# Kernel optimization log

Hardware: AMD Instinct MI355X
Metric: run time of the kernel (lower is better)

Reference implementation:

```python
import jax, jax.numpy as jnp
import numpy as np

P, N, M = 4, 8192, 8192

def setup_inputs() -> dict:
    key = jax.random.key(0)
    k1, k2, k3, k4, k5 = jax.random.split(key, 5)
    return {
        "camera_pts": jax.random.normal(k1, (P, N, 3), dtype=jnp.float32),
        "cad_pts": jax.random.normal(k2, (P, M, 3), dtype=jnp.float32),
        "part_weight": jax.random.uniform(k3, (P,), dtype=jnp.float32),
        "rot_quat": jax.random.normal(k4, (P, 4), dtype=jnp.float32),
        "tra": jax.random.normal(k5, (P, 3, 1), dtype=jnp.float32),
    }

def _quat_to_rot(q):
    # q: [P,4] in (w,x,y,z) order, normalized outside
    a, b, c, d = q[:, 0], q[:, 1], q[:, 2], q[:, 3]
    rows = jnp.stack([
        1 - 2*c*c - 2*d*d, 2*b*c - 2*a*d,     2*a*c + 2*b*d,
        2*b*c + 2*a*d,     1 - 2*b*b - 2*d*d, 2*c*d - 2*a*b,
        2*b*d - 2*a*c,     2*a*b + 2*c*d,     1 - 2*b*b - 2*c*c,
    ], axis=-1)  # [P,9]
    return rows.reshape(-1, 3, 3)

def _chamfer(x, y):
    # x: [N,4], y: [M,4] -> scalar bidirectional chamfer (Euclidean, not squared)
    x2 = jnp.sum(x * x, axis=-1)              # [N]
    y2 = jnp.sum(y * y, axis=-1)              # [M]
    d2 = x2[:, None] + y2[None, :] - 2.0 * (x @ y.T)
    dist = jnp.sqrt(jnp.clip(d2, 0.0))        # [N,M]
    return jnp.mean(jnp.min(dist, axis=1)) + jnp.mean(jnp.min(dist, axis=0))

def reference(camera_pts, cad_pts, part_weight, rot_quat, tra):
    q = rot_quat / jnp.linalg.norm(rot_quat, axis=1, keepdims=True)
    rot = _quat_to_rot(q)                                       # [P,3,3]
    top = jnp.concatenate([rot, tra], axis=2)                   # [P,3,4]
    bottom = jnp.broadcast_to(jnp.array([[[0.0, 0.0, 0.0, 1.0]]], dtype=rot.dtype), (rot.shape[0], 1, 4))
    transforms = jnp.concatenate([top, bottom], axis=1)         # [P,4,4]
    ones_cad = jnp.ones(cad_pts.shape[:-1] + (1,), dtype=cad_pts.dtype)
    ones_cam = jnp.ones(camera_pts.shape[:-1] + (1,), dtype=camera_pts.dtype)
    cad_h = jnp.concatenate([cad_pts, ones_cad], axis=-1)       # [P,M,4]
    cam_h = jnp.concatenate([camera_pts, ones_cam], axis=-1)    # [P,N,4]
    cad_base = jnp.einsum('pij,pmj->pmi', transforms, cad_h)    # [P,M,4]
    cd = jax.vmap(_chamfer)(cad_base, cam_h)                    # [P]
    all_objective = jnp.sum(part_weight * cd)
    return all_objective, jax.lax.stop_gradient(transforms)
```

## Files before the change

kernel.cpp:

```cpp
#include <hip/hip_runtime.h>
#include <math.h>

#define NP 4
#define NN 8192
#define NM 8192

#define TQ 16
#define QT 4096
#define SPLITS 64
#define SPAN 128
#define NPAIR (SPAN / 2)

typedef float float2v __attribute__((ext_vector_type(2)));
typedef float float4v __attribute__((ext_vector_type(4)));

__device__ inline float min3f(float a, float b, float c) {
    float d;
    asm("v_min3_f32 %0, %1, %2, %3" : "=v"(d) : "v"(a), "v"(b), "v"(c));
    return d;
}

__device__ inline float2v pk_fma_blo(float2v a, float2v b, float2v c) {
    float2v d;
    asm("v_pk_fma_f32 %0, %1, %2, %3 op_sel:[0,0,0] op_sel_hi:[0,1,1]"
        : "=v"(d) : "v"(a), "v"(b), "v"(c));
    return d;
}

__device__ inline float2v pk_fma_bhi(float2v a, float2v b, float2v c) {
    float2v d;
    asm("v_pk_fma_f32 %0, %1, %2, %3 op_sel:[1,0,0] op_sel_hi:[1,1,1]"
        : "=v"(d) : "v"(a), "v"(b), "v"(c));
    return d;
}

__device__ inline void make_transform(const float* __restrict__ quat,
                                      const float* __restrict__ tra,
                                      int p, float T[12]) {
    float q0 = quat[p * 4 + 0], q1 = quat[p * 4 + 1];
    float q2 = quat[p * 4 + 2], q3 = quat[p * 4 + 3];
    float inv = 1.0f / sqrtf(q0 * q0 + q1 * q1 + q2 * q2 + q3 * q3);
    float a = q0 * inv, b = q1 * inv, c = q2 * inv, d = q3 * inv;
    T[0] = 1.0f - 2.0f * c * c - 2.0f * d * d;
    T[1] = 2.0f * b * c - 2.0f * a * d;
    T[2] = 2.0f * a * c + 2.0f * b * d;
    T[3] = tra[p * 3 + 0];
    T[4] = 2.0f * b * c + 2.0f * a * d;
    T[5] = 1.0f - 2.0f * b * b - 2.0f * d * d;
    T[6] = 2.0f * c * d - 2.0f * a * b;
    T[7] = tra[p * 3 + 1];
    T[8] = 2.0f * b * d - 2.0f * a * c;
    T[9] = 2.0f * a * b + 2.0f * c * d;
    T[10] = 1.0f - 2.0f * b * b - 2.0f * c * c;
    T[11] = tra[p * 3 + 2];
}

__global__ __launch_bounds__(256, 4)
void chamfer_kernel(const float* __restrict__ cam, const float* __restrict__ cad,
                    const float* __restrict__ quat, const float* __restrict__ tra,
                    float* __restrict__ mins_f, float* __restrict__ out) {
    int tid = threadIdx.x;
    int p = blockIdx.z >> 1;
    int role = blockIdx.z & 1;

    float T[12];
    make_transform(quat, tra, p, T);

    if (blockIdx.x == 0 && blockIdx.y == 0 && blockIdx.z == 0) {
        if (tid < 64) {
            int p2 = tid >> 4;
            int r = (tid >> 2) & 3;
            int c = tid & 3;
            float T2[12];
            make_transform(quat, tra, p2, T2);
            float v;
            if (r == 3)
                v = (c == 3) ? 1.0f : 0.0f;
            else
                v = T2[r * 4 + c];
            out[1 + tid] = v;
        } else if (tid == 64) {
            out[0] = 0.0f;
        }
    }

    __shared__ float sQf[SPAN * 4];
    if (tid < SPAN) {
        const float* src = (role ? cad : cam) +
                           ((size_t)p * 8192 + blockIdx.y * SPAN + tid) * 3;
        float x = src[0], y = src[1], z = src[2];
        float vx, vy, vz;
        if (role) {
            vx = fmaf(T[0], x, fmaf(T[1], y, fmaf(T[2], z, T[3])));
            vy = fmaf(T[4], x, fmaf(T[5], y, fmaf(T[6], z, T[7])));
            vz = fmaf(T[8], x, fmaf(T[9], y, fmaf(T[10], z, T[11])));
        } else {
            vx = x; vy = y; vz = z;
        }
        float h = 0.5f * (vx * vx + vy * vy + vz * vz);
        int lane = tid & 1;
        int f = (tid & ~1) * 4;
        sQf[f + lane] = vx;
        sQf[f + 2 + lane] = vy;
        sQf[f + 4 + lane] = vz;
        sQf[f + 6 + lane] = h;
    }

    const float INF = __uint_as_float(0x7f800000u);
    int q0 = blockIdx.x * QT + tid;
    const float* qbase = (role ? cam : cad) + (size_t)p * 8192 * 3;
    float2v A[TQ], B[TQ];
    float tmin[TQ];
#pragma unroll
    for (int k = 0; k < TQ; ++k) {
        const float* s = qbase + (size_t)(q0 + k * 256) * 3;
        float x = s[0], y = s[1], z = s[2];
        float vx, vy, vz;
        if (!role) {
            vx = fmaf(T[0], x, fmaf(T[1], y, fmaf(T[2], z, T[3])));
            vy = fmaf(T[4], x, fmaf(T[5], y, fmaf(T[6], z, T[7])));
            vz = fmaf(T[8], x, fmaf(T[9], y, fmaf(T[10], z, T[11])));
        } else {
            vx = x; vy = y; vz = z;
        }
        float h = 0.5f * (vx * vx + vy * vy + vz * vz);
        A[k] = (float2v){-vx, -vy};
        B[k] = (float2v){-vz, h};
        tmin[k] = INF;
    }
    __syncthreads();

    const float4v* sQd = (const float4v*)sQf;
    float4v xy0 = sQd[0], zh0 = sQd[1];
#pragma unroll 2
    for (int pp = 0; pp < NPAIR; ++pp) {
        int pn = (pp + 1) & (NPAIR - 1);
        float4v xy1 = sQd[2 * pn];
        float4v zh1 = sQd[2 * pn + 1];

        float2v X = __builtin_shufflevector(xy0, xy0, 0, 1);
        float2v Y = __builtin_shufflevector(xy0, xy0, 2, 3);
        float2v Z = __builtin_shufflevector(zh0, zh0, 0, 1);
        float2v H = __builtin_shufflevector(zh0, zh0, 2, 3);
#pragma unroll
        for (int k = 0; k < TQ; ++k) {
            float2v t = pk_fma_blo(B[k], Z, H);
            t = pk_fma_bhi(A[k], Y, t);
            t = pk_fma_blo(A[k], X, t);
            tmin[k] = min3f(tmin[k], t.x, t.y);
        }
        xy0 = xy1;
        zh0 = zh1;
    }

    unsigned int* mins = (unsigned int*)mins_f + (size_t)blockIdx.z * 8192;
#pragma unroll
    for (int k = 0; k < TQ; ++k) {
        float d2 = 2.0f * (B[k].y + tmin[k]);
        d2 = fmaxf(d2, 0.0f);
        atomicMin(&mins[q0 + k * 256], __float_as_uint(d2));
    }
}

__global__ __launch_bounds__(256) void finalize_kernel(
    const float* __restrict__ mins, const float* __restrict__ w,
    float* __restrict__ out) {
    int i = blockIdx.x * 256 + threadIdx.x;
    int tid = threadIdx.x;

    float m = mins[i];
    float acc = w[i >> 14] * sqrtf(m);

#pragma unroll
    for (int off = 32; off > 0; off >>= 1) acc += __shfl_down(acc, off, 64);

    __shared__ float wsum[4];
    if ((tid & 63) == 0) wsum[tid >> 6] = acc;
    __syncthreads();
    if (tid == 0) {
        float blocksum = (wsum[0] + wsum[1] + wsum[2] + wsum[3]) * (1.0f / 8192.0f);
        atomicAdd(out, blocksum);
    }
}

extern "C" void kernel_launch(void* const* d_in, const int* in_sizes, int n_in,
                              void* d_out, int out_size, void* d_ws, size_t ws_size,
                              hipStream_t stream) {
    const float* cam = (const float*)d_in[0];
    const float* cad = (const float*)d_in[1];
    const float* w = (const float*)d_in[2];
    const float* quat = (const float*)d_in[3];
    const float* tra = (const float*)d_in[4];
    float* out = (float*)d_out;
    float* ws = (float*)d_ws;

    hipMemsetAsync(ws, 0x7f, (size_t)65536 * sizeof(float), stream);

    dim3 grid(NM / QT, SPLITS, 2 * NP);
    chamfer_kernel<<<grid, 256, 0, stream>>>(cam, cad, quat, tra, ws, out);

    finalize_kernel<<<256, 256, 0, stream>>>(ws, w, out);
}
```

Measured before the change: 114.0 us.

## Precompute transformed reference points in a prep kernel and drop LDS staging

Adds a prep kernel that transforms all points once, stores (-2x,-2y,-2z,|v|^2) per point in workspace, initializes the min buffer and writes the transform output. This replaces the memset and the per-block LDS staging. The chamfer inner loop now reads reference points directly from global memory as float4 and uses scalar FMAs instead of hand-written packed FMA. It removes the barrier and LDS traffic but may double FMA issue count if the compiler does not repack, and it adds a kernel launch.

```diff
diff --git a/kernel.cpp b/kernel.cpp
--- a/kernel.cpp
+++ b/kernel.cpp
@@ -5,32 +5,17 @@
 #define NN 8192
 #define NM 8192
 
+#define TP_OFF   0
+#define MINS_OFF 524288
+
 #define TQ 16
 #define QT 4096
 #define SPLITS 64
 #define SPAN 128
-#define NPAIR (SPAN / 2)
-
-typedef float float2v __attribute__((ext_vector_type(2)));
-typedef float float4v __attribute__((ext_vector_type(4)));
 
 __device__ inline float min3f(float a, float b, float c) {
     float d;
     asm("v_min3_f32 %0, %1, %2, %3" : "=v"(d) : "v"(a), "v"(b), "v"(c));
-    return d;
-}
-
-__device__ inline float2v pk_fma_blo(float2v a, float2v b, float2v c) {
-    float2v d;
-    asm("v_pk_fma_f32 %0, %1, %2, %3 op_sel:[0,0,0] op_sel_hi:[0,1,1]"
-        : "=v"(d) : "v"(a), "v"(b), "v"(c));
-    return d;
-}
-
-__device__ inline float2v pk_fma_bhi(float2v a, float2v b, float2v c) {
-    float2v d;
-    asm("v_pk_fma_f32 %0, %1, %2, %3 op_sel:[1,0,0] op_sel_hi:[1,1,1]"
-        : "=v"(d) : "v"(a), "v"(b), "v"(c));
     return d;
 }
 
@@ -55,109 +40,106 @@
     T[11] = tra[p * 3 + 2];
 }
 
+__global__ __launch_bounds__(256) void prep_kernel(
+    const float* __restrict__ cam, const float* __restrict__ cad,
+    const float* __restrict__ quat, const float* __restrict__ tra,
+    float* __restrict__ ws, float* __restrict__ out) {
+    int idx = blockIdx.x * 256 + threadIdx.x;
+    int i = idx & 8191;
+    int p = (idx >> 13) & 3;
+    bool is_cad = idx < 32768;
+
+    const float* src = (is_cad ? cad : cam) + ((size_t)p * 8192 + i) * 3;
+    float x = src[0], y = src[1], z = src[2];
+    float vx, vy, vz;
+    if (is_cad) {
+        float T[12];
+        make_transform(quat, tra, p, T);
+        vx = fmaf(T[0], x, fmaf(T[1], y, fmaf(T[2], z, T[3])));
+        vy = fmaf(T[4], x, fmaf(T[5], y, fmaf(T[6], z, T[7])));
+        vz = fmaf(T[8], x, fmaf(T[9], y, fmaf(T[10], z, T[11])));
+    } else {
+        vx = x; vy = y; vz = z;
+    }
+    float nrm = vx * vx + vy * vy + vz * vz;
+
+    int zt = is_cad ? 2 * p + 1 : 2 * p;
+    ((float4*)(ws + TP_OFF))[(size_t)zt * 8192 + i] =
+        make_float4(-2.0f * vx, -2.0f * vy, -2.0f * vz, nrm);
+
+    ((unsigned int*)(ws + MINS_OFF))[idx] = 0x7f800000u;
+
+    if (idx < 64) {
+        int p2 = idx >> 4;
+        int rr = (idx >> 2) & 3;
+        int c = idx & 3;
+        float T2[12];
+        make_transform(quat, tra, p2, T2);
+        float v;
+        if (rr == 3)
+            v = (c == 3) ? 1.0f : 0.0f;
+        else
+            v = T2[rr * 4 + c];
+        out[1 + idx] = v;
+    } else if (idx == 64) {
+        out[0] = 0.0f;
+    }
+}
+
 __global__ __launch_bounds__(256, 4)
 void chamfer_kernel(const float* __restrict__ cam, const float* __restrict__ cad,
                     const float* __restrict__ quat, const float* __restrict__ tra,
-                    float* __restrict__ mins_f, float* __restrict__ out) {
+                    float* __restrict__ ws) {
     int tid = threadIdx.x;
-    int p = blockIdx.z >> 1;
-    int role = blockIdx.z & 1;
+    int z = blockIdx.z;
+    int p = z >> 1;
+    int role = z & 1;
 
     float T[12];
     make_transform(quat, tra, p, T);
-
-    if (blockIdx.x == 0 && blockIdx.y == 0 && blockIdx.z == 0) {
-        if (tid < 64) {
-            int p2 = tid >> 4;
-            int r = (tid >> 2) & 3;
-            int c = tid & 3;
-            float T2[12];
-            make_transform(quat, tra, p2, T2);
-            float v;
-            if (r == 3)
-                v = (c == 3) ? 1.0f : 0.0f;
-            else
-                v = T2[r * 4 + c];
-            out[1 + tid] = v;
-        } else if (tid == 64) {
-            out[0] = 0.0f;
-        }
-    }
-
-    __shared__ float sQf[SPAN * 4];
-    if (tid < SPAN) {
-        const float* src = (role ? cad : cam) +
-                           ((size_t)p * 8192 + blockIdx.y * SPAN + tid) * 3;
-        float x = src[0], y = src[1], z = src[2];
-        float vx, vy, vz;
-        if (role) {
-            vx = fmaf(T[0], x, fmaf(T[1], y, fmaf(T[2], z, T[3])));
-            vy = fmaf(T[4], x, fmaf(T[5], y, fmaf(T[6], z, T[7])));
-            vz = fmaf(T[8], x, fmaf(T[9], y, fmaf(T[10], z, T[11])));
-        } else {
-            vx = x; vy = y; vz = z;
-        }
-        float h = 0.5f * (vx * vx + vy * vy + vz * vz);
-        int lane = tid & 1;
-        int f = (tid & ~1) * 4;
-        sQf[f + lane] = vx;
-        sQf[f + 2 + lane] = vy;
-        sQf[f + 4 + lane] = vz;
-        sQf[f + 6 + lane] = h;
-    }
-
-    const float INF = __uint_as_float(0x7f800000u);
     int q0 = blockIdx.x * QT + tid;
     const float* qbase = (role ? cam : cad) + (size_t)p * 8192 * 3;
-    float2v A[TQ], B[TQ];
-    float tmin[TQ];
+    float qx[TQ], qy[TQ], qz[TQ], hq[TQ], tmin[TQ];
+    const float INF = __uint_as_float(0x7f800000u);
 #pragma unroll
     for (int k = 0; k < TQ; ++k) {
         const float* s = qbase + (size_t)(q0 + k * 256) * 3;
-        float x = s[0], y = s[1], z = s[2];
+        float x = s[0], y = s[1], zz = s[2];
         float vx, vy, vz;
         if (!role) {
-            vx = fmaf(T[0], x, fmaf(T[1], y, fmaf(T[2], z, T[3])));
-            vy = fmaf(T[4], x, fmaf(T[5], y, fmaf(T[6], z, T[7])));
-            vz = fmaf(T[8], x, fmaf(T[9], y, fmaf(T[10], z, T[11])));
+            vx = fmaf(T[0], x, fmaf(T[1], y, fmaf(T[2], zz, T[3])));
+            vy = fmaf(T[4], x, fmaf(T[5], y, fmaf(T[6], zz, T[7])));
+            vz = fmaf(T[8], x, fmaf(T[9], y, fmaf(T[10], zz, T[11])));
         } else {
-            vx = x; vy = y; vz = z;
+            vx = x; vy = y; vz = zz;
         }
-        float h = 0.5f * (vx * vx + vy * vy + vz * vz);
-        A[k] = (float2v){-vx, -vy};
-        B[k] = (float2v){-vz, h};
+        qx[k] = vx; qy[k] = vy; qz[k] = vz;
+        hq[k] = vx * vx + vy * vy + vz * vz;
         tmin[k] = INF;
     }
-    __syncthreads();
 
-    const float4v* sQd = (const float4v*)sQf;
-    float4v xy0 = sQd[0], zh0 = sQd[1];
+    const float4* TPz = (const float4*)(ws + TP_OFF) + (size_t)z * 8192 +
+                        blockIdx.y * SPAN;
 #pragma unroll 2
-    for (int pp = 0; pp < NPAIR; ++pp) {
-        int pn = (pp + 1) & (NPAIR - 1);
-        float4v xy1 = sQd[2 * pn];
-        float4v zh1 = sQd[2 * pn + 1];
-
-        float2v X = __builtin_shufflevector(xy0, xy0, 0, 1);
-        float2v Y = __builtin_shufflevector(xy0, xy0, 2, 3);
-        float2v Z = __builtin_shufflevector(zh0, zh0, 0, 1);
-        float2v H = __builtin_shufflevector(zh0, zh0, 2, 3);
+    for (int g = 0; g < SPAN / 2; ++g) {
+        float4 t0 = TPz[2 * g];
+        float4 t1 = TPz[2 * g + 1];
+        float a0[TQ], a1[TQ];
 #pragma unroll
-        for (int k = 0; k < TQ; ++k) {
-            float2v t = pk_fma_blo(B[k], Z, H);
-            t = pk_fma_bhi(A[k], Y, t);
-            t = pk_fma_blo(A[k], X, t);
-            tmin[k] = min3f(tmin[k], t.x, t.y);
-        }
-        xy0 = xy1;
-        zh0 = zh1;
+        for (int k = 0; k < TQ; ++k)
+            a0[k] = fmaf(t0.z, qz[k], fmaf(t0.y, qy[k], fmaf(t0.x, qx[k], t0.w)));
+#pragma unroll
+        for (int k = 0; k < TQ; ++k)
+            a1[k] = fmaf(t1.z, qz[k], fmaf(t1.y, qy[k], fmaf(t1.x, qx[k], t1.w)));
+#pragma unroll
+        for (int k = 0; k < TQ; ++k)
+            tmin[k] = min3f(tmin[k], a0[k], a1[k]);
     }
 
-    unsigned int* mins = (unsigned int*)mins_f + (size_t)blockIdx.z * 8192;
+    unsigned int* mins = (unsigned int*)(ws + MINS_OFF) + (size_t)z * 8192;
 #pragma unroll
     for (int k = 0; k < TQ; ++k) {
-        float d2 = 2.0f * (B[k].y + tmin[k]);
-        d2 = fmaxf(d2, 0.0f);
+        float d2 = fmaxf(hq[k] + tmin[k], 0.0f);
         atomicMin(&mins[q0 + k * 256], __float_as_uint(d2));
     }
 }
@@ -194,10 +176,10 @@
     float* out = (float*)d_out;
     float* ws = (float*)d_ws;
 
-    hipMemsetAsync(ws, 0x7f, (size_t)65536 * sizeof(float), stream);
+    prep_kernel<<<256, 256, 0, stream>>>(cam, cad, quat, tra, ws, out);
 
     dim3 grid(NM / QT, SPLITS, 2 * NP);
-    chamfer_kernel<<<grid, 256, 0, stream>>>(cam, cad, quat, tra, ws, out);
+    chamfer_kernel<<<grid, 256, 0, stream>>>(cam, cad, quat, tra, ws);
 
-    finalize_kernel<<<256, 256, 0, stream>>>(ws, w, out);
+    finalize_kernel<<<256, 256, 0, stream>>>(ws + MINS_OFF, w, out);
 }
```

Result: slower. 132.5 us (+16.2%).
